# Kernel tuning notes

Measured on AMD Instinct MI355X. Metric: run time of the kernel, lower is better.

The kernel has to match this reference:

```python
import jax, jax.numpy as jnp
import numpy as np

N_LOC, N_EVT, E = 100000, 200000, 1000000
F_LOC, F_EVT, H = 128, 128, 64


def setup_inputs() -> dict:
    key = jax.random.key(0)
    ks = jax.random.split(key, 12)
    s = lambda k, shp: jax.random.normal(k, shp, dtype=jnp.float32) * (1.0 / np.sqrt(shp[0]))
    return {
        "loc_x": jax.random.normal(ks[0], (N_LOC, F_LOC), dtype=jnp.float32),
        "evt_x": jax.random.normal(ks[1], (N_EVT, F_EVT), dtype=jnp.float32),
        "edge_index": jax.random.randint(ks[2], (2, E), 0, N_LOC, dtype=jnp.int64),
        # projections (stored as (in, out))
        "W_loc": s(ks[3], (F_LOC, H)), "b_loc": jnp.zeros((H,), jnp.float32),
        "W_evt": s(ks[4], (F_EVT, H)), "b_evt": jnp.zeros((H,), jnp.float32),
        # SAGEConv: lin_l (on aggregated src, with bias), lin_r (on dst root, no bias)
        "W_l": s(ks[5], (H, H)), "b_l": jnp.zeros((H,), jnp.float32),
        "W_r": s(ks[6], (H, H)),
        # head MLP
        "W_h1": s(ks[7], (H, H // 2)), "b_h1": jnp.zeros((H // 2,), jnp.float32),
        "W_h2": s(ks[8], (H // 2, 1)), "b_h2": jnp.zeros((1,), jnp.float32),
    }


def reference(loc_x, evt_x, edge_index, W_loc, b_loc, W_evt, b_evt,
              W_l, b_l, W_r, W_h1, b_h1, W_h2, b_h2):
    # node projections + ReLU
    loc_h = jax.nn.relu(loc_x @ W_loc + b_loc)   # [N_loc, H]
    evt_h = jax.nn.relu(evt_x @ W_evt + b_evt)   # [N_evt, H]

    src, dst = edge_index[0], edge_index[1]      # event -> location
    n_loc = loc_h.shape[0]
    # mean aggregation of source (event) features onto destination (location) nodes
    msg_sum = jax.ops.segment_sum(evt_h[src], dst, num_segments=n_loc)   # [N_loc, H]
    cnt = jax.ops.segment_sum(jnp.ones_like(dst, dtype=loc_h.dtype), dst,
                              num_segments=n_loc)
    agg = msg_sum / jnp.maximum(cnt, 1.0)[:, None]
    # SAGEConv: lin_l(agg) + lin_r(root), then ReLU
    loc_h = jax.nn.relu(agg @ W_l + b_l + loc_h @ W_r)

    # prediction head
    h = jax.nn.relu(loc_h @ W_h1 + b_h1)
    logits = (h @ W_h2 + b_h2)[:, 0]             # [N_loc]
    return logits
```

## Files before the change

### kernel.cpp

```cpp
#include <hip/hip_runtime.h>


#define N_LOC 100000
#define N_EVT 200000
#define E_CNT 1000000
#define NTILES 6250
#define NBKT   256
#define BKT_L  391
#define CAPG   6000
#define QCAP   32
#define PERB   7813

typedef __attribute__((ext_vector_type(8))) short short8;
typedef __attribute__((ext_vector_type(4))) float floatx4;

__device__ __forceinline__ float b2f(unsigned short u) {
    unsigned int x = ((unsigned int)u) << 16;
    return __builtin_bit_cast(float, x);
}
__device__ __forceinline__ unsigned short f2b(float f) {
    unsigned int x = __builtin_bit_cast(unsigned int, f);
    unsigned int r = (x + 0x7fffu + ((x >> 16) & 1u)) >> 16;
    return (unsigned short)r;
}
__device__ __forceinline__ float loadf(const void* p, int f32, size_t i) {
    return f32 ? ((const float*)p)[i] : b2f(((const unsigned short*)p)[i]);
}

__global__ __launch_bounds__(256) void prep_kernel(
    const void* t0, const void* t1, const int* eidx,
    const void* t3, const void* t4, const void* t5, const void* t6,
    const void* t7, const void* t8, const void* t9, const void* t10,
    const void* t11, const void* t12, const void* t13,
    int* flags, int* gbc, unsigned short* __restrict__ wp_all) {
    int b = blockIdx.x, tid = threadIdx.x;
    __shared__ int s0, s1;

    if (b == 14) { gbc[tid] = 0; return; }

    if (b >= 15) {
        int pb = b - 15;
        const void* W; int K, N, bstart, off;
        if (pb < 4)       { W = t5;  K = 128; N = 64; bstart = 0;  off = 0; }
        else if (pb < 8)  { W = t3;  K = 128; N = 64; bstart = 4;  off = 8192; }
        else if (pb < 10) { W = t7;  K = 64;  N = 64; bstart = 8;  off = 16384; }
        else if (pb < 12) { W = t9;  K = 64;  N = 64; bstart = 10; off = 20480; }
        else              { W = t10; K = 64;  N = 32; bstart = 12; off = 24576; }
        if (tid == 0) s0 = 0;
        __syncthreads();
        int nsamp = 2 * K * N; if (nsamp > 1024) nsamp = 1024;
        const unsigned short* h = (const unsigned short*)W;
        int susp = 0;
        for (int i = tid; i < nsamp; i += 256)
            if (((h[i] >> 7) & 0xFF) >= 0x90) susp++;
        if (susp) atomicAdd(&s0, susp);
        __syncthreads();
        int f32 = (s0 * 16 >= nsamp) ? 1 : 0;

        int idx  = (pb - bstart) * 256 + tid;
        int nk   = K >> 5;
        int f    = idx >> 6;
        int lane = idx & 63;
        int t  = f / nk;
        int kk = f - t * nk;
        int n  = t * 16 + (lane & 15);
        int k0 = kk * 32 + (lane >> 4) * 8;
        unsigned short tmp[8];
#pragma unroll
        for (int j = 0; j < 8; ++j) {
            size_t src = (size_t)(k0 + j) * N + n;
            tmp[j] = f32 ? f2b(((const float*)W)[src])
                         : ((const unsigned short*)W)[src];
        }
#pragma unroll
        for (int j = 0; j < 8; ++j) wp_all[(size_t)off + (size_t)idx * 8 + j] = tmp[j];
        return;
    }

    if (tid == 0) { s0 = 0; s1 = 0; }
    __syncthreads();
    if (b == 13) {
        if (tid < 128) {
            if (eidx[2 * tid] != 0) atomicAdd(&s0, 1);
            if (eidx[2 * tid + 1] != 0) atomicAdd(&s1, 1);
        }
        __syncthreads();
        if (tid == 0) flags[2] = (s1 == 0 && s0 > 32) ? 1 : 0;
        return;
    }
    const void* ptrs[13] = {t0, t1, t3, t4, t5, t6, t7, t8, t9, t10, t11, t12, t13};
    const int   cnts[13] = {12800000, 25600000, 8192, 64, 8192, 64,
                            4096, 64, 4096, 2048, 32, 32, 1};
    const int   slot[13] = {0, 1, 3, 4, 5, 6, 7, 8, 9, 10, 11, 12, 13};
    int nsamp = 2 * cnts[b];
    if (nsamp > 1024) nsamp = 1024;
    const unsigned short* h = (const unsigned short*)ptrs[b];
    int susp = 0;
    for (int i = tid; i < nsamp; i += 256)
        if (((h[i] >> 7) & 0xFF) >= 0x90) susp++;
    if (susp) atomicAdd(&s0, susp);
    __syncthreads();
    if (tid == 0) flags[slot[b]] = (s0 * 16 >= nsamp) ? 1 : 0;
}

__global__ __launch_bounds__(256) void proj_both_kernel(
    const void* __restrict__ evt_x, const void* __restrict__ loc_x,
    const unsigned short* __restrict__ wp_all,
    const void* __restrict__ b_evt, const void* __restrict__ b_loc,
    unsigned short* __restrict__ evt_h, unsigned short* __restrict__ loc_h,
    const int* __restrict__ flags) {
    int blk = blockIdx.x;
    const void* X; const unsigned short* Wp; const void* bias;
    unsigned short* Y; int M, fx, fb, bb;
    if (blk < 3125) { X = evt_x; Wp = wp_all;        bias = b_evt; Y = evt_h;
                      M = N_EVT; fx = flags[1]; fb = flags[6]; bb = blk; }
    else            { X = loc_x; Wp = wp_all + 8192; bias = b_loc; Y = loc_h;
                      M = N_LOC; fx = flags[0]; fb = flags[4]; bb = blk - 3125; }
    int tid  = threadIdx.x;
    int lane = tid & 63;
    int wv   = tid >> 6;
    int l15  = lane & 15;
    int quad = lane >> 4;
    int row_base = bb * 64 + wv * 16;

    short8 b[16];
#pragma unroll
    for (int f = 0; f < 16; ++f)
        b[f] = *reinterpret_cast<const short8*>(Wp + ((size_t)(f * 64 + lane)) * 8);

    int m = row_base + l15;
    short8 a[4];
#pragma unroll
    for (int kk = 0; kk < 4; ++kk) a[kk] = (short8)0;
    if (m < M) {
        if (fx) {
            const float* xr = (const float*)X + (size_t)m * 128 + quad * 8;
#pragma unroll
            for (int kk = 0; kk < 4; ++kk) {
                float4 p0 = *reinterpret_cast<const float4*>(xr + kk * 32);
                float4 p1 = *reinterpret_cast<const float4*>(xr + kk * 32 + 4);
                short8 v;
                v[0] = (short)f2b(p0.x); v[1] = (short)f2b(p0.y);
                v[2] = (short)f2b(p0.z); v[3] = (short)f2b(p0.w);
                v[4] = (short)f2b(p1.x); v[5] = (short)f2b(p1.y);
                v[6] = (short)f2b(p1.z); v[7] = (short)f2b(p1.w);
                a[kk] = v;
            }
        } else {
            const unsigned short* xr = (const unsigned short*)X + (size_t)m * 128 + quad * 8;
#pragma unroll
            for (int kk = 0; kk < 4; ++kk)
                a[kk] = *reinterpret_cast<const short8*>(xr + kk * 32);
        }
    }

    floatx4 acc[4];
#pragma unroll
    for (int t = 0; t < 4; ++t) acc[t] = (floatx4)0.0f;
#pragma unroll
    for (int kk = 0; kk < 4; ++kk) {
#pragma unroll
        for (int t = 0; t < 4; ++t)
            acc[t] = __builtin_amdgcn_mfma_f32_16x16x32_bf16(
                a[kk], b[t * 4 + kk], acc[t], 0, 0, 0);
    }

#pragma unroll
    for (int t = 0; t < 4; ++t) {
        float bv = loadf(bias, fb, t * 16 + l15);
#pragma unroll
        for (int r = 0; r < 4; ++r) {
            int row = row_base + quad * 4 + r;
            if (row < M) {
                float v = acc[t][r] + bv;
                v = v > 0.0f ? v : 0.0f;
                Y[(size_t)row * 64 + t * 16 + l15] = f2b(v);
            }
        }
    }
}

__global__ __launch_bounds__(256) void bucket_kernel(
    const int* __restrict__ eidx, uint2* __restrict__ bkt,
    int* __restrict__ gbc, const int* __restrict__ flags) {
    __shared__ uint2 queue[NBKT][QCAP];
    __shared__ int qcnt[NBKT];
    int tid = threadIdx.x, blk = blockIdx.x;
    qcnt[tid] = 0;
    __syncthreads();
    int f64 = flags[2];
    const long long* e64 = (const long long*)eidx;
    int e0 = blk * PERB;
    int e1 = e0 + PERB; if (e1 > E_CNT) e1 = E_CNT;
    const int rounds = (PERB + 255) / 256;

    for (int r = 0; r < rounds; ++r) {
        int e = e0 + r * 256 + tid;
        if (e < e1) {
            int src, dst;
            if (f64) { src = (int)e64[e]; dst = (int)e64[E_CNT + e]; }
            else     { src = eidx[e];     dst = eidx[E_CNT + e]; }
            if ((unsigned)dst < (unsigned)N_LOC && (unsigned)src < (unsigned)N_EVT) {
                int bk = dst / BKT_L;
                int pos = atomicAdd(&qcnt[bk], 1);
                if (pos < QCAP) {
                    queue[bk][pos] = make_uint2((unsigned)src, (unsigned)dst);
                } else {
                    int p = atomicAdd(&gbc[bk], 1);
                    if (p < CAPG) bkt[(size_t)bk * CAPG + p] = make_uint2(src, dst);
                }
            }
        }
        __syncthreads();
        int n = qcnt[tid]; if (n > QCAP) n = QCAP;
        while (n >= 16) {
            int gp = atomicAdd(&gbc[tid], 16);
            if (gp + 16 <= CAPG) {
                uint2* d = bkt + (size_t)tid * CAPG + gp;
#pragma unroll
                for (int j = 0; j < 16; ++j) d[j] = queue[tid][j];
            }
#pragma unroll
            for (int j = 16; j < QCAP; ++j) queue[tid][j - 16] = queue[tid][j];
            n -= 16;
        }
        qcnt[tid] = n;
        __syncthreads();
    }
    int n = qcnt[tid]; if (n > QCAP) n = QCAP;
    if (n > 0) {
        int gp = atomicAdd(&gbc[tid], n);
        for (int j = 0; j < n; ++j)
            if (gp + j < CAPG) bkt[(size_t)tid * CAPG + gp + j] = queue[tid][j];
    }
}

__global__ void scan_gbc_kernel(const int* __restrict__ gbc,
                                int* __restrict__ bbase) {
    __shared__ int sh[256];
    int t = threadIdx.x;
    int v = gbc[t]; if (v > CAPG) v = CAPG;
    sh[t] = v;
    __syncthreads();
    for (int d = 1; d < 256; d <<= 1) {
        int x = (t >= d) ? sh[t - d] : 0;
        __syncthreads();
        sh[t] += x;
        __syncthreads();
    }
    bbase[t] = sh[t] - v;
}

__global__ __launch_bounds__(256) void csr_build_kernel(
    const uint2* __restrict__ bkt, const int* __restrict__ gbc,
    const int* __restrict__ bbase,
    int* __restrict__ rowptr, int* __restrict__ csr) {
    __shared__ int lcnt[512];
    __shared__ int lscan[512];
    __shared__ int lcsr[CAPG];
    int b = blockIdx.x, tid = threadIdx.x;
    int loc0 = b * BKT_L;
    int nloc = N_LOC - loc0; if (nloc > BKT_L) nloc = BKT_L;
    int cntE = gbc[b]; if (cntE > CAPG) cntE = CAPG;
    int base = bbase[b];
    const uint2* bp = bkt + (size_t)b * CAPG;

    int i0 = tid, i1 = tid + 256;
    lcnt[i0] = 0; lcnt[i1] = 0;
    __syncthreads();
    for (int i = tid; i < cntE; i += 256) {
        int d = (int)bp[i].y - loc0;
        atomicAdd(&lcnt[d], 1);
    }
    __syncthreads();
    lscan[i0] = lcnt[i0]; lscan[i1] = lcnt[i1];
    __syncthreads();
    for (int d = 1; d < 512; d <<= 1) {
        int v0 = (i0 >= d) ? lscan[i0 - d] : 0;
        int v1 = (i1 >= d) ? lscan[i1 - d] : 0;
        __syncthreads();
        lscan[i0] += v0; lscan[i1] += v1;
        __syncthreads();
    }
    for (int i = tid; i < nloc; i += 256) {
        int excl = lscan[i] - lcnt[i];
        rowptr[loc0 + i] = base + excl;
        lcnt[i] = excl;
    }
    if (b == NBKT - 1 && tid == 0) rowptr[N_LOC] = base + cntE;
    __syncthreads();
    for (int i = tid; i < cntE; i += 256) {
        uint2 pr = bp[i];
        int d = (int)pr.y - loc0;
        int p = atomicAdd(&lcnt[d], 1);
        if (p < CAPG) lcsr[p] = (int)pr.x;
    }
    __syncthreads();
    for (int i = tid; i < cntE; i += 256) csr[base + i] = lcsr[i];
}

__global__ __launch_bounds__(256) void aggregate_kernel(
    const unsigned short* __restrict__ evt_h,
    const int* __restrict__ rowptr, const int* __restrict__ csr,
    unsigned short* __restrict__ agg, int N) {
    int wid  = (blockIdx.x * 256 + threadIdx.x) >> 6;
    int lane = threadIdx.x & 63;
    if (wid >= N) return;
    int e0 = rowptr[wid], e1 = rowptr[wid + 1];
    float acc = 0.0f;
    for (int j = e0; j < e1; j += 4) {
        int c1 = j + 1 < e1, c2 = j + 2 < e1, c3 = j + 3 < e1;
        int s0 = csr[j];
        int s1 = csr[c1 ? j + 1 : j];
        int s2 = csr[c2 ? j + 2 : j];
        int s3 = csr[c3 ? j + 3 : j];
        float v0 = b2f(evt_h[(size_t)s0 * 64 + lane]);
        float v1 = b2f(evt_h[(size_t)s1 * 64 + lane]);
        float v2 = b2f(evt_h[(size_t)s2 * 64 + lane]);
        float v3 = b2f(evt_h[(size_t)s3 * 64 + lane]);
        acc += v0;
        if (c1) acc += v1;
        if (c2) acc += v2;
        if (c3) acc += v3;
    }
    float inv = (e1 > e0) ? 1.0f / (float)(e1 - e0) : 0.0f;
    agg[(size_t)wid * 64 + lane] = f2b(acc * inv);
}

__global__ __launch_bounds__(256) void head_kernel(
    const unsigned short* __restrict__ agg,
    const unsigned short* __restrict__ loc_h,
    const unsigned short* __restrict__ wp_all,
    const void* __restrict__ bl, const void* __restrict__ bh1,
    const void* __restrict__ wh2, const void* __restrict__ bh2,
    void* __restrict__ out, const int* __restrict__ flags) {
    __shared__ unsigned short h2s[4][16 * 64];
    int tid = threadIdx.x, lane = tid & 63, wv = tid >> 6;
    int tile = blockIdx.x * 4 + wv;
    if (tile >= NTILES) return;
    int l15 = lane & 15, quad = lane >> 4;
    int fbl = flags[8], fbh1 = flags[11], fwh2 = flags[12], fbh2 = flags[13];
    int fout = flags[0];
    int base = tile * 16;
    const unsigned short* wp_l  = wp_all + 16384;
    const unsigned short* wp_r  = wp_all + 20480;
    const unsigned short* wp_h1 = wp_all + 24576;

    short8 bwl[8], bwr[8], bw1[4];
#pragma unroll
    for (int f = 0; f < 8; ++f) {
        bwl[f] = *reinterpret_cast<const short8*>(wp_l + ((size_t)(f * 64 + lane)) * 8);
        bwr[f] = *reinterpret_cast<const short8*>(wp_r + ((size_t)(f * 64 + lane)) * 8);
    }
#pragma unroll
    for (int f = 0; f < 4; ++f)
        bw1[f] = *reinterpret_cast<const short8*>(wp_h1 + ((size_t)(f * 64 + lane)) * 8);

    short8 aA[2], aL[2];
#pragma unroll
    for (int kk = 0; kk < 2; ++kk) {
        aA[kk] = *reinterpret_cast<const short8*>(
            agg + (size_t)(base + l15) * 64 + kk * 32 + quad * 8);
        aL[kk] = *reinterpret_cast<const short8*>(
            loc_h + (size_t)(base + l15) * 64 + kk * 32 + quad * 8);
    }

    floatx4 acc[4];
#pragma unroll
    for (int t = 0; t < 4; ++t) acc[t] = (floatx4)0.0f;
#pragma unroll
    for (int kk = 0; kk < 2; ++kk) {
#pragma unroll
        for (int t = 0; t < 4; ++t) {
            acc[t] = __builtin_amdgcn_mfma_f32_16x16x32_bf16(
                aA[kk], bwl[t * 2 + kk], acc[t], 0, 0, 0);
            acc[t] = __builtin_amdgcn_mfma_f32_16x16x32_bf16(
                aL[kk], bwr[t * 2 + kk], acc[t], 0, 0, 0);
        }
    }

#pragma unroll
    for (int t = 0; t < 4; ++t) {
        float bb = loadf(bl, fbl, t * 16 + l15);
#pragma unroll
        for (int r = 0; r < 4; ++r) {
            float v = acc[t][r] + bb;
            v = v > 0.0f ? v : 0.0f;
            h2s[wv][(quad * 4 + r) * 64 + t * 16 + l15] = f2b(v);
        }
    }
    short8 aH[2];
#pragma unroll
    for (int kk = 0; kk < 2; ++kk)
        aH[kk] = *reinterpret_cast<const short8*>(
            &h2s[wv][l15 * 64 + kk * 32 + quad * 8]);

    floatx4 a1[2];
#pragma unroll
    for (int t = 0; t < 2; ++t) a1[t] = (floatx4)0.0f;
#pragma unroll
    for (int kk = 0; kk < 2; ++kk)
#pragma unroll
        for (int t = 0; t < 2; ++t)
            a1[t] = __builtin_amdgcn_mfma_f32_16x16x32_bf16(
                aH[kk], bw1[t * 2 + kk], a1[t], 0, 0, 0);

    float s[4] = {0.f, 0.f, 0.f, 0.f};
#pragma unroll
    for (int t = 0; t < 2; ++t) {
        float bb = loadf(bh1, fbh1, t * 16 + l15);
        float w2 = loadf(wh2, fwh2, t * 16 + l15);
#pragma unroll
        for (int r = 0; r < 4; ++r) {
            float v = a1[t][r] + bb;
            v = v > 0.0f ? v : 0.0f;
            s[r] += v * w2;
        }
    }
#pragma unroll
    for (int r = 0; r < 4; ++r) {
        s[r] += __shfl_xor(s[r], 1);
        s[r] += __shfl_xor(s[r], 2);
        s[r] += __shfl_xor(s[r], 4);
        s[r] += __shfl_xor(s[r], 8);
    }
    float bb2 = loadf(bh2, fbh2, 0);
#pragma unroll
    for (int r = 0; r < 4; ++r) {
        if (l15 == r) {
            int row = base + quad * 4 + r;
            float v = s[r] + bb2;
            if (fout) ((float*)out)[row] = v;
            else      ((unsigned short*)out)[row] = f2b(v);
        }
    }
}

extern "C" void kernel_launch(void* const* d_in, const int* in_sizes, int n_in,
                              void* d_out, int out_size, void* d_ws, size_t ws_size,
                              hipStream_t stream) {
    (void)in_sizes; (void)n_in; (void)out_size; (void)ws_size;
    const void* loc_x = d_in[0];
    const void* evt_x = d_in[1];
    const int*  eidx  = (const int*)d_in[2];
    const void* W_loc = d_in[3];
    const void* b_loc = d_in[4];
    const void* W_evt = d_in[5];
    const void* b_evt = d_in[6];
    const void* W_l   = d_in[7];
    const void* b_l   = d_in[8];
    const void* W_r   = d_in[9];
    const void* W_h1  = d_in[10];
    const void* b_h1  = d_in[11];
    const void* W_h2  = d_in[12];
    const void* b_h2  = d_in[13];

    char* ws = (char*)d_ws;
    unsigned short* evt_h  = (unsigned short*)(ws);
    unsigned short* loc_h  = (unsigned short*)(ws + 25600000);
    int*            csr    = (int*)(ws + 38400000);
    int*            rowptr = (int*)(ws + 42400000);
    int*            gbc    = (int*)(ws + 42800016);
    int*            bbase  = (int*)(ws + 42801040);
    unsigned short* wp_all = (unsigned short*)(ws + 42802064);
    int*            flags  = (int*)(ws + 42855312);
    uint2*          bkt    = (uint2*)(ws + 42855376);
    unsigned short* agg    = (unsigned short*)(ws + 42855376);

    prep_kernel<<<28, 256, 0, stream>>>(
        loc_x, evt_x, eidx, W_loc, b_loc, W_evt, b_evt,
        W_l, b_l, W_r, W_h1, b_h1, W_h2, b_h2,
        flags, gbc, wp_all);

    proj_both_kernel<<<4688, 256, 0, stream>>>(evt_x, loc_x, wp_all,
                                               b_evt, b_loc, evt_h, loc_h, flags);

    bucket_kernel<<<128, 256, 0, stream>>>(eidx, bkt, gbc, flags);
    scan_gbc_kernel<<<1, 256, 0, stream>>>(gbc, bbase);
    csr_build_kernel<<<NBKT, 256, 0, stream>>>(bkt, gbc, bbase, rowptr, csr);

    aggregate_kernel<<<(N_LOC + 3) / 4, 256, 0, stream>>>(evt_h, rowptr, csr,
                                                          agg, N_LOC);

    head_kernel<<<(NTILES + 3) / 4, 256, 0, stream>>>(
        agg, loc_h, wp_all, b_l, b_h1, W_h2, b_h2, d_out, flags);
}
```

Measured before the change: 352.4 us.

## Make projection and head kernels persistent with software-prefetched tiles; widen bucket grid

The projection and head kernels become persistent grid-stride loops. Each wave loads the weight fragments and biases once, then prefetches the next tile's input rows while it runs MFMA on the current tile, using double buffering in the head kernel. The bucket kernel gets more blocks with fewer edges each, to raise parallelism. The intent is to amortise per-block weight loads and hide global-memory latency, at the cost of higher register pressure and fewer resident blocks.

```diff
diff --git a/kernel.cpp b/kernel.cpp
--- a/kernel.cpp
+++ b/kernel.cpp
@@ -9,7 +9,15 @@
 #define BKT_L  391
 #define CAPG   6000
 #define QCAP   32
-#define PERB   7813
+#define BKT_BLK 512
+#define PERB   1954
+
+#define PROJ_EVT_BLK 512
+#define PROJ_LOC_BLK 256
+#define PROJ_BLK_TOT (PROJ_EVT_BLK + PROJ_LOC_BLK)
+#define EVT_TILES 12500
+#define LOC_TILES 6250
+#define HEAD_BLK  512
 
 typedef __attribute__((ext_vector_type(8))) short short8;
 typedef __attribute__((ext_vector_type(4))) float floatx4;
@@ -103,42 +111,66 @@
     if (tid == 0) flags[slot[b]] = (s0 * 16 >= nsamp) ? 1 : 0;
 }
 
-__global__ __launch_bounds__(256) void proj_both_kernel(
+__global__ __launch_bounds__(256, 3) void proj_both_kernel(
     const void* __restrict__ evt_x, const void* __restrict__ loc_x,
     const unsigned short* __restrict__ wp_all,
     const void* __restrict__ b_evt, const void* __restrict__ b_loc,
     unsigned short* __restrict__ evt_h, unsigned short* __restrict__ loc_h,
     const int* __restrict__ flags) {
     int blk = blockIdx.x;
+    int tid = threadIdx.x, lane = tid & 63, wv = tid >> 6;
+    int l15 = lane & 15, quad = lane >> 4;
+
     const void* X; const unsigned short* Wp; const void* bias;
-    unsigned short* Y; int M, fx, fb, bb;
-    if (blk < 3125) { X = evt_x; Wp = wp_all;        bias = b_evt; Y = evt_h;
-                      M = N_EVT; fx = flags[1]; fb = flags[6]; bb = blk; }
-    else            { X = loc_x; Wp = wp_all + 8192; bias = b_loc; Y = loc_h;
-                      M = N_LOC; fx = flags[0]; fb = flags[4]; bb = blk - 3125; }
-    int tid  = threadIdx.x;
-    int lane = tid & 63;
-    int wv   = tid >> 6;
-    int l15  = lane & 15;
-    int quad = lane >> 4;
-    int row_base = bb * 64 + wv * 16;
+    unsigned short* Y; int fx, fb, w0, nw, ntile;
+    if (blk < PROJ_EVT_BLK) {
+        X = evt_x; Wp = wp_all;        bias = b_evt; Y = evt_h;
+        fx = flags[1]; fb = flags[6];
+        w0 = blk * 4 + wv; nw = PROJ_EVT_BLK * 4; ntile = EVT_TILES;
+    } else {
+        X = loc_x; Wp = wp_all + 8192; bias = b_loc; Y = loc_h;
+        fx = flags[0]; fb = flags[4];
+        w0 = (blk - PROJ_EVT_BLK) * 4 + wv; nw = PROJ_LOC_BLK * 4; ntile = LOC_TILES;
+    }
 
     short8 b[16];
 #pragma unroll
     for (int f = 0; f < 16; ++f)
         b[f] = *reinterpret_cast<const short8*>(Wp + ((size_t)(f * 64 + lane)) * 8);
 
-    int m = row_base + l15;
-    short8 a[4];
-#pragma unroll
-    for (int kk = 0; kk < 4; ++kk) a[kk] = (short8)0;
-    if (m < M) {
+    float bv[4];
+#pragma unroll
+    for (int q = 0; q < 4; ++q) bv[q] = loadf(bias, fb, q * 16 + l15);
+
+    if (w0 >= ntile) return;
+
+    float4 pf[8];
+    short8 an[4];
+
+    auto issue = [&](int t) {
+        int m = t * 16 + l15;
         if (fx) {
             const float* xr = (const float*)X + (size_t)m * 128 + quad * 8;
 #pragma unroll
             for (int kk = 0; kk < 4; ++kk) {
-                float4 p0 = *reinterpret_cast<const float4*>(xr + kk * 32);
-                float4 p1 = *reinterpret_cast<const float4*>(xr + kk * 32 + 4);
+                pf[kk * 2]     = *reinterpret_cast<const float4*>(xr + kk * 32);
+                pf[kk * 2 + 1] = *reinterpret_cast<const float4*>(xr + kk * 32 + 4);
+            }
+        } else {
+            const unsigned short* xr = (const unsigned short*)X + (size_t)m * 128 + quad * 8;
+#pragma unroll
+            for (int kk = 0; kk < 4; ++kk)
+                an[kk] = *reinterpret_cast<const short8*>(xr + kk * 32);
+        }
+    };
+
+    issue(w0);
+    for (int t = w0; t < ntile; t += nw) {
+        short8 a[4];
+        if (fx) {
+#pragma unroll
+            for (int kk = 0; kk < 4; ++kk) {
+                float4 p0 = pf[kk * 2], p1 = pf[kk * 2 + 1];
                 short8 v;
                 v[0] = (short)f2b(p0.x); v[1] = (short)f2b(p0.y);
                 v[2] = (short)f2b(p0.z); v[3] = (short)f2b(p0.w);
@@ -147,36 +179,30 @@
                 a[kk] = v;
             }
         } else {
-            const unsigned short* xr = (const unsigned short*)X + (size_t)m * 128 + quad * 8;
-#pragma unroll
-            for (int kk = 0; kk < 4; ++kk)
-                a[kk] = *reinterpret_cast<const short8*>(xr + kk * 32);
-        }
-    }
-
-    floatx4 acc[4];
-#pragma unroll
-    for (int t = 0; t < 4; ++t) acc[t] = (floatx4)0.0f;
-#pragma unroll
-    for (int kk = 0; kk < 4; ++kk) {
-#pragma unroll
-        for (int t = 0; t < 4; ++t)
-            acc[t] = __builtin_amdgcn_mfma_f32_16x16x32_bf16(
-                a[kk], b[t * 4 + kk], acc[t], 0, 0, 0);
-    }
-
-#pragma unroll
-    for (int t = 0; t < 4; ++t) {
-        float bv = loadf(bias, fb, t * 16 + l15);
-#pragma unroll
-        for (int r = 0; r < 4; ++r) {
-            int row = row_base + quad * 4 + r;
-            if (row < M) {
-                float v = acc[t][r] + bv;
+#pragma unroll
+            for (int kk = 0; kk < 4; ++kk) a[kk] = an[kk];
+        }
+        int tn = t + nw;
+        if (tn < ntile) issue(tn);
+
+        floatx4 acc[4];
+#pragma unroll
+        for (int q = 0; q < 4; ++q) acc[q] = (floatx4)0.0f;
+#pragma unroll
+        for (int kk = 0; kk < 4; ++kk)
+#pragma unroll
+            for (int q = 0; q < 4; ++q)
+                acc[q] = __builtin_amdgcn_mfma_f32_16x16x32_bf16(
+                    a[kk], b[q * 4 + kk], acc[q], 0, 0, 0);
+
+#pragma unroll
+        for (int q = 0; q < 4; ++q)
+#pragma unroll
+            for (int r = 0; r < 4; ++r) {
+                float v = acc[q][r] + bv[q];
                 v = v > 0.0f ? v : 0.0f;
-                Y[(size_t)row * 64 + t * 16 + l15] = f2b(v);
-            }
-        }
+                Y[(size_t)(t * 16 + quad * 4 + r) * 64 + q * 16 + l15] = f2b(v);
+            }
     }
 }
 
@@ -327,7 +353,7 @@
     agg[(size_t)wid * 64 + lane] = f2b(acc * inv);
 }
 
-__global__ __launch_bounds__(256) void head_kernel(
+__global__ __launch_bounds__(256, 3) void head_kernel(
     const unsigned short* __restrict__ agg,
     const unsigned short* __restrict__ loc_h,
     const unsigned short* __restrict__ wp_all,
@@ -336,12 +362,9 @@
     void* __restrict__ out, const int* __restrict__ flags) {
     __shared__ unsigned short h2s[4][16 * 64];
     int tid = threadIdx.x, lane = tid & 63, wv = tid >> 6;
-    int tile = blockIdx.x * 4 + wv;
-    if (tile >= NTILES) return;
     int l15 = lane & 15, quad = lane >> 4;
     int fbl = flags[8], fbh1 = flags[11], fwh2 = flags[12], fbh2 = flags[13];
     int fout = flags[0];
-    int base = tile * 16;
     const unsigned short* wp_l  = wp_all + 16384;
     const unsigned short* wp_r  = wp_all + 20480;
     const unsigned short* wp_h1 = wp_all + 24576;
@@ -356,83 +379,110 @@
     for (int f = 0; f < 4; ++f)
         bw1[f] = *reinterpret_cast<const short8*>(wp_h1 + ((size_t)(f * 64 + lane)) * 8);
 
-    short8 aA[2], aL[2];
-#pragma unroll
-    for (int kk = 0; kk < 2; ++kk) {
-        aA[kk] = *reinterpret_cast<const short8*>(
-            agg + (size_t)(base + l15) * 64 + kk * 32 + quad * 8);
-        aL[kk] = *reinterpret_cast<const short8*>(
-            loc_h + (size_t)(base + l15) * 64 + kk * 32 + quad * 8);
-    }
-
-    floatx4 acc[4];
-#pragma unroll
-    for (int t = 0; t < 4; ++t) acc[t] = (floatx4)0.0f;
-#pragma unroll
-    for (int kk = 0; kk < 2; ++kk) {
-#pragma unroll
-        for (int t = 0; t < 4; ++t) {
-            acc[t] = __builtin_amdgcn_mfma_f32_16x16x32_bf16(
-                aA[kk], bwl[t * 2 + kk], acc[t], 0, 0, 0);
-            acc[t] = __builtin_amdgcn_mfma_f32_16x16x32_bf16(
-                aL[kk], bwr[t * 2 + kk], acc[t], 0, 0, 0);
-        }
-    }
-
-#pragma unroll
-    for (int t = 0; t < 4; ++t) {
-        float bb = loadf(bl, fbl, t * 16 + l15);
+    float bbl[4], bh1v[2], w2v[2];
+#pragma unroll
+    for (int q = 0; q < 4; ++q) bbl[q] = loadf(bl, fbl, q * 16 + l15);
+#pragma unroll
+    for (int q = 0; q < 2; ++q) {
+        bh1v[q] = loadf(bh1, fbh1, q * 16 + l15);
+        w2v[q]  = loadf(wh2, fwh2, q * 16 + l15);
+    }
+    float bb2 = loadf(bh2, fbh2, 0);
+
+    const int NW = HEAD_BLK * 4;
+    int w0 = blockIdx.x * 4 + wv;
+    if (w0 >= NTILES) return;
+
+    short8 c0[4], c1[4];
+
+    auto issue = [&](short8* c, int t) {
+        int m = t * 16 + l15;
+#pragma unroll
+        for (int kk = 0; kk < 2; ++kk) {
+            c[kk]     = *reinterpret_cast<const short8*>(
+                agg + (size_t)m * 64 + kk * 32 + quad * 8);
+            c[2 + kk] = *reinterpret_cast<const short8*>(
+                loc_h + (size_t)m * 64 + kk * 32 + quad * 8);
+        }
+    };
+
+    auto compute = [&](const short8* c, int tile) {
+        floatx4 acc[4];
+#pragma unroll
+        for (int q = 0; q < 4; ++q) acc[q] = (floatx4)0.0f;
+#pragma unroll
+        for (int kk = 0; kk < 2; ++kk)
+#pragma unroll
+            for (int q = 0; q < 4; ++q) {
+                acc[q] = __builtin_amdgcn_mfma_f32_16x16x32_bf16(
+                    c[kk], bwl[q * 2 + kk], acc[q], 0, 0, 0);
+                acc[q] = __builtin_amdgcn_mfma_f32_16x16x32_bf16(
+                    c[2 + kk], bwr[q * 2 + kk], acc[q], 0, 0, 0);
+            }
+#pragma unroll
+        for (int q = 0; q < 4; ++q)
+#pragma unroll
+            for (int r = 0; r < 4; ++r) {
+                float v = acc[q][r] + bbl[q];
+                v = v > 0.0f ? v : 0.0f;
+                h2s[wv][(quad * 4 + r) * 64 + q * 16 + l15] = f2b(v);
+            }
+        short8 aH[2];
+#pragma unroll
+        for (int kk = 0; kk < 2; ++kk)
+            aH[kk] = *reinterpret_cast<const short8*>(
+                &h2s[wv][l15 * 64 + kk * 32 + quad * 8]);
+
+        floatx4 a1[2];
+#pragma unroll
+        for (int q = 0; q < 2; ++q) a1[q] = (floatx4)0.0f;
+#pragma unroll
+        for (int kk = 0; kk < 2; ++kk)
+#pragma unroll
+            for (int q = 0; q < 2; ++q)
+                a1[q] = __builtin_amdgcn_mfma_f32_16x16x32_bf16(
+                    aH[kk], bw1[q * 2 + kk], a1[q], 0, 0, 0);
+
+        float s[4] = {0.f, 0.f, 0.f, 0.f};
+#pragma unroll
+        for (int q = 0; q < 2; ++q)
+#pragma unroll
+            for (int r = 0; r < 4; ++r) {
+                float v = a1[q][r] + bh1v[q];
+                v = v > 0.0f ? v : 0.0f;
+                s[r] += v * w2v[q];
+            }
 #pragma unroll
         for (int r = 0; r < 4; ++r) {
-            float v = acc[t][r] + bb;
-            v = v > 0.0f ? v : 0.0f;
-            h2s[wv][(quad * 4 + r) * 64 + t * 16 + l15] = f2b(v);
-        }
-    }
-    short8 aH[2];
-#pragma unroll
-    for (int kk = 0; kk < 2; ++kk)
-        aH[kk] = *reinterpret_cast<const short8*>(
-            &h2s[wv][l15 * 64 + kk * 32 + quad * 8]);
-
-    floatx4 a1[2];
-#pragma unroll
-    for (int t = 0; t < 2; ++t) a1[t] = (floatx4)0.0f;
-#pragma unroll
-    for (int kk = 0; kk < 2; ++kk)
-#pragma unroll
-        for (int t = 0; t < 2; ++t)
-            a1[t] = __builtin_amdgcn_mfma_f32_16x16x32_bf16(
-                aH[kk], bw1[t * 2 + kk], a1[t], 0, 0, 0);
-
-    float s[4] = {0.f, 0.f, 0.f, 0.f};
-#pragma unroll
-    for (int t = 0; t < 2; ++t) {
-        float bb = loadf(bh1, fbh1, t * 16 + l15);
-        float w2 = loadf(wh2, fwh2, t * 16 + l15);
+            s[r] += __shfl_xor(s[r], 1);
+            s[r] += __shfl_xor(s[r], 2);
+            s[r] += __shfl_xor(s[r], 4);
+            s[r] += __shfl_xor(s[r], 8);
+        }
 #pragma unroll
         for (int r = 0; r < 4; ++r) {
-            float v = a1[t][r] + bb;
-            v = v > 0.0f ? v : 0.0f;
-            s[r] += v * w2;
-        }
-    }
-#pragma unroll
-    for (int r = 0; r < 4; ++r) {
-        s[r] += __shfl_xor(s[r], 1);
-        s[r] += __shfl_xor(s[r], 2);
-        s[r] += __shfl_xor(s[r], 4);
-        s[r] += __shfl_xor(s[r], 8);
-    }
-    float bb2 = loadf(bh2, fbh2, 0);
-#pragma unroll
-    for (int r = 0; r < 4; ++r) {
-        if (l15 == r) {
-            int row = base + quad * 4 + r;
-            float v = s[r] + bb2;
-            if (fout) ((float*)out)[row] = v;
-            else      ((unsigned short*)out)[row] = f2b(v);
-        }
+            if (l15 == r) {
+                int row = tile * 16 + quad * 4 + r;
+                float v = s[r] + bb2;
+                if (fout) ((float*)out)[row] = v;
+                else      ((unsigned short*)out)[row] = f2b(v);
+            }
+        }
+    };
+
+    issue(c0, w0);
+    int t = w0;
+    while (true) {
+        int tn = t + NW;
+        bool hn = tn < NTILES;
+        if (hn) issue(c1, tn);
+        compute(c0, t);
+        if (!hn) break;
+        t = tn; tn = t + NW; hn = tn < NTILES;
+        if (hn) issue(c0, tn);
+        compute(c1, t);
+        if (!hn) break;
+        t = tn;
     }
 }
 
@@ -472,16 +522,16 @@
         W_l, b_l, W_r, W_h1, b_h1, W_h2, b_h2,
         flags, gbc, wp_all);
 
-    proj_both_kernel<<<4688, 256, 0, stream>>>(evt_x, loc_x, wp_all,
-                                               b_evt, b_loc, evt_h, loc_h, flags);
-
-    bucket_kernel<<<128, 256, 0, stream>>>(eidx, bkt, gbc, flags);
+    proj_both_kernel<<<PROJ_BLK_TOT, 256, 0, stream>>>(
+        evt_x, loc_x, wp_all, b_evt, b_loc, evt_h, loc_h, flags);
+
+    bucket_kernel<<<BKT_BLK, 256, 0, stream>>>(eidx, bkt, gbc, flags);
     scan_gbc_kernel<<<1, 256, 0, stream>>>(gbc, bbase);
     csr_build_kernel<<<NBKT, 256, 0, stream>>>(bkt, gbc, bbase, rowptr, csr);
 
     aggregate_kernel<<<(N_LOC + 3) / 4, 256, 0, stream>>>(evt_h, rowptr, csr,
                                                           agg, N_LOC);
 
-    head_kernel<<<(NTILES + 3) / 4, 256, 0, stream>>>(
+    head_kernel<<<HEAD_BLK, 256, 0, stream>>>(
         agg, loc_h, wp_all, b_l, b_h1, W_h2, b_h2, d_out, flags);
 }
```

New measurement: 321.7 us. 8.7% less time.
